# Kernel optimization log

Hardware: AMD Instinct MI355X
Metric: run time of the kernel (lower is better)

The kernel has to match this reference:

```python
import jax, jax.numpy as jnp
import numpy as np

Q_HEADS, KV_HEADS, HEAD_SIZE, H, MAX_LEN = 16, 4, 64, 1024, 4096
B, S = 1, 4096


def _rope_tables(max_len, head_size):
    half = head_size // 2
    inv_freq = 1.0 / (10000.0 ** (np.arange(half, dtype=np.float32) / half))
    pos = np.arange(max_len, dtype=np.float32)
    ang = pos[:, None] * inv_freq[None, :]  # [max_len, half]
    return jnp.asarray(np.sin(ang)), jnp.asarray(np.cos(ang))


def setup_inputs() -> dict:
    key = jax.random.key(0)
    ks = jax.random.split(key, 6)
    sc = 1.0 / np.sqrt(H)
    x = jax.random.normal(ks[0], (B, S, H), dtype=jnp.float32)
    wq = jax.random.normal(ks[1], (H, H), dtype=jnp.float32) * sc
    wk = jax.random.normal(ks[2], (H, KV_HEADS * HEAD_SIZE), dtype=jnp.float32) * sc
    wv = jax.random.normal(ks[3], (H, KV_HEADS * HEAD_SIZE), dtype=jnp.float32) * sc
    wo = jax.random.normal(ks[4], (H, H), dtype=jnp.float32) * sc
    sin, cos = _rope_tables(MAX_LEN, HEAD_SIZE)
    full_mask = jnp.tril(jnp.ones((MAX_LEN, MAX_LEN), dtype=bool))
    attention_mask = jnp.ones((B, S), dtype=jnp.int32)
    return {"x": x, "attention_mask": attention_mask, "start": 0,
            "wq": wq, "wk": wk, "wv": wv, "wo": wo,
            "sin": sin, "cos": cos, "full_mask": full_mask}


def _rotate(t, sin, cos, start):
    # t: [b, heads, s, head_size]; interleaved even/odd RoPE
    s = t.shape[2]
    sn = sin[start:start + s, :][None, None, :, :]
    cs = cos[start:start + s, :][None, None, :, :]
    even, odd = t[..., 0::2], t[..., 1::2]
    out_even = cs * even - sn * odd
    out_odd = sn * even + cs * odd
    return jnp.stack((out_even, out_odd), axis=-1).reshape(t.shape)


def _expand_kv(t, group):
    # [b, kv_heads, s, d] -> [b, kv_heads*group, s, d]
    b, kvh, s, d = t.shape
    return jnp.broadcast_to(t[:, :, None], (b, kvh, group, s, d)).reshape(b, kvh * group, s, d)


def reference(x, attention_mask, start, wq, wk, wv, wo, sin, cos, full_mask):
    b, s, _ = x.shape
    group = Q_HEADS // KV_HEADS
    Q = (x @ wq).reshape(b, s, Q_HEADS, HEAD_SIZE).transpose(0, 2, 1, 3)
    K = (x @ wk).reshape(b, s, KV_HEADS, HEAD_SIZE).transpose(0, 2, 1, 3)
    V = (x @ wv).reshape(b, s, KV_HEADS, HEAD_SIZE).transpose(0, 2, 1, 3)
    Q = _rotate(Q, sin, cos, start)
    K = _rotate(K, sin, cos, start)
    K = _expand_kv(K, group)
    V = _expand_kv(V, group)
    z = jnp.einsum('bhqd,bhkd->bhqk', Q, K) / (HEAD_SIZE ** 0.5)
    kv_len = start + s
    mask = full_mask[:s, :kv_len][None, None, :, :]
    amask = (attention_mask[:, :kv_len] != 0)[:, None, None, :]
    mask = mask & amask
    z = jnp.where(mask, z, -1000000.0)
    A = jax.nn.softmax(z, axis=-1)
    ctx = jnp.einsum('bhqk,bhkd->bhqd', A, V)
    q_mask = attention_mask[:, :s].astype(ctx.dtype)[:, None, :, None]
    ctx = ctx * q_mask
    ctx = ctx.transpose(0, 2, 1, 3).reshape(b, s, H)
    return ctx @ wo
```

## Files before the change

kernel.cpp:

```cpp
#include <hip/hip_runtime.h>

typedef __bf16 bf16x8 __attribute__((ext_vector_type(8)));
typedef float f32x4 __attribute__((ext_vector_type(4)));
typedef unsigned int u32x4 __attribute__((ext_vector_type(4)));

typedef const void __attribute__((address_space(1)))* gas1;
typedef void __attribute__((address_space(3)))* las3;

__device__ __forceinline__ unsigned short f2bf(float f) {
  unsigned int u = __builtin_bit_cast(unsigned int, f);
  u += 0x7fffu + ((u >> 16) & 1u);
  return (unsigned short)(u >> 16);
}
__device__ __forceinline__ float bf2f(unsigned short h) {
  unsigned int u = ((unsigned int)h) << 16;
  return __builtin_bit_cast(float, u);
}
__device__ __forceinline__ unsigned int pack2bf(float lo, float hi) {
  return (unsigned int)f2bf(lo) | ((unsigned int)f2bf(hi) << 16);
}
__device__ __forceinline__ unsigned int packtr(float lo, float hi) {
  return __builtin_amdgcn_perm(__builtin_bit_cast(unsigned int, hi),
                               __builtin_bit_cast(unsigned int, lo), 0x07060302u);
}

__global__ __launch_bounds__(256) void prep(const float* __restrict__ x,
                                            const float* __restrict__ wq,
                                            const float* __restrict__ wk,
                                            const float* __restrict__ wv,
                                            const float* __restrict__ wo,
                                            const float* __restrict__ sinT,
                                            const float* __restrict__ cosT,
                                            unsigned short* __restrict__ xb,
                                            unsigned short* __restrict__ wtqkv,
                                            unsigned short* __restrict__ wot,
                                            float2* __restrict__ scT) {
  __shared__ float tile[32][33];
  const int b = blockIdx.x;
  const int tid = threadIdx.x;
  if (b < 4096) {
    int i = b * 256 + tid;
    float4 v = ((const float4*)x)[i];
    uint2 o;
    o.x = pack2bf(v.x, v.y);
    o.y = pack2bf(v.z, v.w);
    ((uint2*)xb)[i] = o;
    return;
  }
  if (b >= 6656) {
    int idx = (b - 6656) * 256 + tid;
    scT[idx] = make_float2(sinT[idx], cosT[idx]);
    return;
  }
  const float* src;
  unsigned short* dst;
  int R, C, t;
  if (b < 5120)      { t = b - 4096; src = wq; dst = wtqkv;               R = 1024; C = 1024; }
  else if (b < 5376) { t = b - 5120; src = wk; dst = wtqkv + 1024 * 1024; R = 1024; C = 256; }
  else if (b < 5632) { t = b - 5376; src = wv; dst = wtqkv + 1280 * 1024; R = 1024; C = 256; }
  else               { t = b - 5632; src = wo; dst = wot;                 R = 1024; C = 1024; }
  const int ntc = C >> 5;
  const int c0 = (t % ntc) * 32, r0 = (t / ntc) * 32;
  const int tx = tid & 31, ty = tid >> 5;
#pragma unroll
  for (int i = 0; i < 4; ++i)
    tile[ty + i * 8][tx] = src[(r0 + ty + i * 8) * C + c0 + tx];
  __syncthreads();
#pragma unroll
  for (int i = 0; i < 4; ++i)
    dst[(c0 + ty + i * 8) * R + r0 + tx] = f2bf(tile[tx][ty + i * 8]);
}


__device__ __forceinline__ void stage_tile(const unsigned short* __restrict__ src,
                                           unsigned short* lds, int tid) {
  const int w = tid >> 6;
  const int l = tid & 63;
  const int rsub = l >> 3;
  const int cblk = l & 7;
#pragma unroll
  for (int i = 0; i < 4; ++i) {
    const int row = i * 32 + w * 8 + rsub;
    const int scol = (cblk ^ (row & 7)) * 8;
    __builtin_amdgcn_global_load_lds((gas1)(const void*)&src[(size_t)row * 1024 + scol],
                                     (las3)(void*)&lds[(i * 32 + w * 8) * 64], 16, 0, 0);
  }
}

#define GEMM_STEP(CUR, NXT, KNEXT, DO_STAGE)                                          \
  {                                                                                   \
    if (DO_STAGE) {                                                                   \
      stage_tile(Ab + (KNEXT), sm[NXT][0], tid);                                      \
      stage_tile(Bb + (KNEXT), sm[NXT][1], tid);                                      \
    }                                                                                 \
    const char* As = (const char*)sm[CUR][0];                                         \
    const char* Bs = (const char*)sm[CUR][1];                                         \
    bf16x8 af[2][4], bfr[2][4];                                                       \
    _Pragma("unroll")                                                                 \
    for (int kk = 0; kk < 2; ++kk) {                                                  \
      const int co = (kk * 64 + lgrp * 16) ^ xorsel;                                  \
      _Pragma("unroll")                                                               \
      for (int mi = 0; mi < 4; ++mi)                                                  \
        af[kk][mi] = __builtin_bit_cast(bf16x8,                                       \
            *(const u32x4*)(As + arow + mi * 2048 + co));                             \
      _Pragma("unroll")                                                               \
      for (int ni = 0; ni < 4; ++ni)                                                  \
        bfr[kk][ni] = __builtin_bit_cast(bf16x8,                                      \
            *(const u32x4*)(Bs + brow + ni * 2048 + co));                             \
    }                                                                                 \
    _Pragma("unroll")                                                                 \
    for (int kk = 0; kk < 2; ++kk)                                                    \
      _Pragma("unroll")                                                               \
      for (int mi = 0; mi < 4; ++mi)                                                  \
        _Pragma("unroll")                                                             \
        for (int ni = 0; ni < 4; ++ni)                                                \
          acc[mi][ni] = __builtin_amdgcn_mfma_f32_16x16x32_bf16(af[kk][mi],           \
                            bfr[kk][ni], acc[mi][ni], 0, 0, 0);                       \
    __syncthreads();                                                                  \
  }

__global__ __launch_bounds__(256, 2) void gemm_qkv(const unsigned short* __restrict__ A,
                                                   const unsigned short* __restrict__ Bt,
                                                   const float2* __restrict__ scT,
                                                   unsigned short* __restrict__ Qh,
                                                   unsigned short* __restrict__ Kh,
                                                   unsigned short* __restrict__ Vt) {
  __shared__ __align__(16) unsigned short sm[2][2][128 * 64];
  const int tid = threadIdx.x;
  const int bid = blockIdx.x;
  const int swz = (bid & 7) * 48 + (bid >> 3);
  const int nt = swz % 12, mt = swz / 12;
  const int m0 = mt * 128, n0 = nt * 128;

  const int lane = tid & 63, wid = tid >> 6;
  const int wr = wid >> 1, wc = wid & 1;
  const int lgrp = lane >> 4, lmod = lane & 15;
  const int xorsel = (lmod & 7) << 4;
  const int arow = (wr * 64 + lmod) * 128;
  const int brow = (wc * 64 + lmod) * 128;

  const unsigned short* Ab = A + (size_t)m0 * 1024;
  const unsigned short* Bb = Bt + (size_t)n0 * 1024;

  f32x4 acc[4][4] = {};

  stage_tile(Ab, sm[0][0], tid);
  stage_tile(Bb, sm[0][1], tid);
  __syncthreads();

  for (int t = 0; t < 16; t += 2) {
    GEMM_STEP(0, 1, (size_t)(t + 1) * 64, true);
    GEMM_STEP(1, 0, (size_t)(t + 2) * 64, t < 14);
  }

  const int ncol0 = n0 + wc * 64;
  if (ncol0 >= 1280) {
    const int kvh = (ncol0 - 1280) >> 6;
#pragma unroll
    for (int mi = 0; mi < 4; ++mi)
#pragma unroll
      for (int ni = 0; ni < 4; ++ni) {
        int d = ni * 16 + lmod;
        int s = m0 + wr * 64 + mi * 16 + lgrp * 4;
        uint2 o;
        o.x = pack2bf(acc[mi][ni][0], acc[mi][ni][1]);
        o.y = pack2bf(acc[mi][ni][2], acc[mi][ni][3]);
        *(uint2*)&Vt[((size_t)(kvh * 64 + d)) * 4096 + s] = o;
      }
    return;
  }

  const float qscale = 0.18033688011112042f;
  const bool isQ = (ncol0 < 1024);
  const int h = isQ ? (ncol0 >> 6) : ((ncol0 - 1024) >> 6);
  unsigned short* dstbase = isQ ? Qh : Kh;
  const bool evn = (lmod & 1) == 0;
#pragma unroll
  for (int mi = 0; mi < 4; ++mi)
#pragma unroll
    for (int ni = 0; ni < 4; ++ni) {
      int d = ni * 16 + lmod;
      int i = d >> 1;
#pragma unroll
      for (int r = 0; r < 4; ++r) {
        float v = acc[mi][ni][r];
        float pp = __shfl_xor(v, 1, 64);
        int row = m0 + wr * 64 + mi * 16 + lgrp * 4 + r;
        float2 sc = scT[(size_t)row * 32 + i];
        float e = evn ? v : pp, o = evn ? pp : v;
        float outv = evn ? (sc.y * e - sc.x * o) : (sc.x * e + sc.y * o);
        if (isQ) outv *= qscale;
        dstbase[((size_t)h * 4096 + row) * 64 + d] = f2bf(outv);
      }
    }
}

__global__ __launch_bounds__(256, 2) void gemm_out(const unsigned short* __restrict__ A,
                                                   const unsigned short* __restrict__ Bt,
                                                   float* __restrict__ Cout) {
  __shared__ __align__(16) unsigned short sm[2][2][128 * 64];
  const int tid = threadIdx.x;
  const int bid = blockIdx.x;
  const int swz = (bid & 7) * 32 + (bid >> 3);
  const int nt = swz & 7, mt = swz >> 3;
  const int m0 = mt * 128, n0 = nt * 128;

  const int lane = tid & 63, wid = tid >> 6;
  const int wr = wid >> 1, wc = wid & 1;
  const int lgrp = lane >> 4, lmod = lane & 15;
  const int xorsel = (lmod & 7) << 4;
  const int arow = (wr * 64 + lmod) * 128;
  const int brow = (wc * 64 + lmod) * 128;

  const unsigned short* Ab = A + (size_t)m0 * 1024;
  const unsigned short* Bb = Bt + (size_t)n0 * 1024;

  f32x4 acc[4][4] = {};

  stage_tile(Ab, sm[0][0], tid);
  stage_tile(Bb, sm[0][1], tid);
  __syncthreads();

  for (int t = 0; t < 16; t += 2) {
    GEMM_STEP(0, 1, (size_t)(t + 1) * 64, true);
    GEMM_STEP(1, 0, (size_t)(t + 2) * 64, t < 14);
  }

#pragma unroll
  for (int mi = 0; mi < 4; ++mi)
#pragma unroll
    for (int ni = 0; ni < 4; ++ni)
#pragma unroll
      for (int r = 0; r < 4; ++r) {
        int row = m0 + wr * 64 + mi * 16 + lgrp * 4 + r;
        int col = n0 + wc * 64 + ni * 16 + lmod;
        Cout[(size_t)row * 1024 + col] = acc[mi][ni][r];
      }
}

__global__ __launch_bounds__(256, 4) void attn6(const unsigned short* __restrict__ Qh,
                                                const unsigned short* __restrict__ Kh,
                                                const unsigned short* __restrict__ Vt,
                                                unsigned short* __restrict__ ctx) {
  __shared__ __align__(16) unsigned short Kls[128 * 64];
  __shared__ __align__(16) unsigned short Vls[64 * 128];
  const int bx = blockIdx.x;
  const int head = bx & 15;
  const int qidx = bx >> 4;
  const int qh = (qidx < 32) ? (63 - qidx) : (qidx - 32);
  const int kvh = head >> 2;
  const int tid = threadIdx.x;
  const int wave = tid >> 6, lane = tid & 63;
  const int lgrp = lane >> 4, lmod = lane & 15;
  const int qbase = qh * 64;
  const int ntile = qh >> 1;

  const unsigned short* Kg = Kh + (size_t)kvh * 4096 * 64;
  const unsigned short* Vg = Vt + (size_t)kvh * 64 * 4096;

  const int qrow = qbase + wave * 16 + lmod;
  const unsigned short* Qg = Qh + ((size_t)head * 4096 + qrow) * 64;
  bf16x8 qf0 = __builtin_bit_cast(bf16x8, *(const u32x4*)&Qg[lgrp * 8]);
  bf16x8 qf1 = __builtin_bit_cast(bf16x8, *(const u32x4*)&Qg[32 + lgrp * 8]);

  f32x4 accO[4] = {};
  float m_i = -3e38f, l_i = 0.f;

  for (int kc = 0; kc <= ntile; ++kc) {
    const int kb = kc * 128;
    __syncthreads();
#pragma unroll
    for (int i = 0; i < 4; ++i) {
      int ii = tid + i * 256;
      int r = ii >> 3, b = ii & 7;
      __builtin_amdgcn_global_load_lds(
          (gas1)(const void*)&Kg[(size_t)(kb + r) * 64 + ((b ^ (r & 7)) * 8)],
          (las3)(void*)&Kls[(size_t)ii * 8], 16, 0, 0);
    }
#pragma unroll
    for (int i = 0; i < 4; ++i) {
      int ii = tid + i * 256;
      int d = ii >> 4, b = ii & 15;
      __builtin_amdgcn_global_load_lds(
          (gas1)(const void*)&Vg[(size_t)d * 4096 + kb + ((b ^ (d & 15)) * 8)],
          (las3)(void*)&Vls[(size_t)ii * 8], 16, 0, 0);
    }
    __syncthreads();

    f32x4 s[4][2];
    __builtin_amdgcn_s_setprio(1);
#pragma unroll
    for (int g = 0; g < 4; ++g)
#pragma unroll
      for (int t = 0; t < 2; ++t) {
        const int row = 32 * g + t + 2 * lmod;
        bf16x8 alo = __builtin_bit_cast(bf16x8,
            *(const u32x4*)&Kls[(size_t)row * 64 + ((lgrp ^ (row & 7)) * 8)]);
        bf16x8 ahi = __builtin_bit_cast(bf16x8,
            *(const u32x4*)&Kls[(size_t)row * 64 + (((4 + lgrp) ^ (row & 7)) * 8)]);
        f32x4 z = {};
        z = __builtin_amdgcn_mfma_f32_16x16x32_bf16(alo, qf0, z, 0, 0, 0);
        z = __builtin_amdgcn_mfma_f32_16x16x32_bf16(ahi, qf1, z, 0, 0, 0);
        s[g][t] = z;
      }
    __builtin_amdgcn_s_setprio(0);

    if (kb + 127 > qbase + wave * 16) {
#pragma unroll
      for (int g = 0; g < 4; ++g)
#pragma unroll
        for (int t = 0; t < 2; ++t)
#pragma unroll
          for (int r = 0; r < 4; ++r) {
            int key = kb + 32 * g + 8 * lgrp + 2 * r + t;
            if (key > qrow) s[g][t][r] = -3e38f;
          }
    }

    {
      f32x4 v0 = s[0][0], v1 = s[0][1];
#pragma unroll
      for (int g = 1; g < 4; ++g)
#pragma unroll
        for (int r = 0; r < 4; ++r) {
          v0[r] = fmaxf(v0[r], s[g][0][r]);
          v1[r] = fmaxf(v1[r], s[g][1][r]);
        }
      float mx = fmaxf(fmaxf(fmaxf(v0[0], v0[1]), fmaxf(v0[2], v0[3])),
                       fmaxf(fmaxf(v1[0], v1[1]), fmaxf(v1[2], v1[3])));
      mx = fmaxf(mx, __shfl_xor(mx, 16, 64));
      mx = fmaxf(mx, __shfl_xor(mx, 32, 64));
      float mnew = fmaxf(m_i, mx);
      float alpha = __builtin_amdgcn_exp2f(m_i - mnew);
      m_i = mnew;
      f32x4 su = {};
#pragma unroll
      for (int g = 0; g < 4; ++g)
#pragma unroll
        for (int t = 0; t < 2; ++t)
#pragma unroll
          for (int r = 0; r < 4; ++r) {
            float ev = __builtin_amdgcn_exp2f(s[g][t][r] - mnew);
            s[g][t][r] = ev;
            su[r] += ev;
          }
      float rs = (su[0] + su[1]) + (su[2] + su[3]);
      rs += __shfl_xor(rs, 16, 64);
      rs += __shfl_xor(rs, 32, 64);
      l_i = l_i * alpha + rs;
#pragma unroll
      for (int dt = 0; dt < 4; ++dt)
#pragma unroll
        for (int r = 0; r < 4; ++r) accO[dt][r] *= alpha;
    }

    __builtin_amdgcn_s_setprio(1);
#pragma unroll
    for (int g = 0; g < 4; ++g) {
      u32x4 pk;
      pk[0] = packtr(s[g][0][0], s[g][1][0]);
      pk[1] = packtr(s[g][0][1], s[g][1][1]);
      pk[2] = packtr(s[g][0][2], s[g][1][2]);
      pk[3] = packtr(s[g][0][3], s[g][1][3]);
      bf16x8 pf = __builtin_bit_cast(bf16x8, pk);
#pragma unroll
      for (int dt = 0; dt < 4; ++dt) {
        const int d = dt * 16 + lmod;
        bf16x8 vf = __builtin_bit_cast(bf16x8,
            *(const u32x4*)&Vls[(size_t)d * 128 + (((4 * g + lgrp) ^ lmod) * 8)]);
        accO[dt] = __builtin_amdgcn_mfma_f32_16x16x32_bf16(vf, pf, accO[dt], 0, 0, 0);
      }
    }
    __builtin_amdgcn_s_setprio(0);
  }

  {
    float inv = 1.f / l_i;
#pragma unroll
    for (int dt = 0; dt < 4; ++dt) {
      uint2 o;
      o.x = pack2bf(accO[dt][0] * inv, accO[dt][1] * inv);
      o.y = pack2bf(accO[dt][2] * inv, accO[dt][3] * inv);
      *(uint2*)&ctx[(size_t)qrow * 1024 + head * 64 + dt * 16 + lgrp * 4] = o;
    }
  }
}

extern "C" void kernel_launch(void* const* d_in, const int* in_sizes, int n_in,
                              void* d_out, int out_size, void* d_ws, size_t ws_size,
                              hipStream_t stream) {
  const float* x    = (const float*)d_in[0];
  const float* wq   = (const float*)d_in[3];
  const float* wk   = (const float*)d_in[4];
  const float* wv   = (const float*)d_in[5];
  const float* wo   = (const float*)d_in[6];
  const float* sinT = (const float*)d_in[7];
  const float* cosT = (const float*)d_in[8];

  unsigned short* ws    = (unsigned short*)d_ws;
  unsigned short* xb    = ws;
  unsigned short* wtqkv = xb + 4096 * 1024;
  unsigned short* wot   = wtqkv + 1536 * 1024;
  unsigned short* Qh    = wot + 1024 * 1024;
  unsigned short* Kh    = Qh + 16 * 4096 * 64;
  unsigned short* Vt    = Kh + 4 * 4096 * 64;
  unsigned short* ctx   = Vt + 4 * 64 * 4096;
  float2* scT           = (float2*)(ctx + 4096 * 1024);
  float* out = (float*)d_out;

  prep<<<7168, 256, 0, stream>>>(x, wq, wk, wv, wo, sinT, cosT, xb, wtqkv, wot, scT);
  gemm_qkv<<<384, 256, 0, stream>>>(xb, wtqkv, scT, Qh, Kh, Vt);
  attn6<<<dim3(1024), 256, 0, stream>>>(Qh, Kh, Vt, ctx);
  gemm_out<<<256, 256, 0, stream>>>(ctx, wot, out);
}
```

Before: 216.2 us.

## Split causal attention across two KV halves with a combine pass

Adds an attention kernel that uses 128-row query tiles and splits each tile's causal key range into two halves handled by separate blocks. Each block writes unnormalized partial outputs plus row max and sum to fp32 workspace, and a new combine kernel merges the two halves and writes bf16 context. The aim is to balance per-block work and raise parallelism for the long causal tiles. The cost is an extra kernel launch and extra fp32 partial traffic through global memory. The old path is kept as a fallback when the workspace is too small.

```diff
diff --git a/kernel.cpp b/kernel.cpp
--- a/kernel.cpp
+++ b/kernel.cpp
@@ -11,10 +11,6 @@
   unsigned int u = __builtin_bit_cast(unsigned int, f);
   u += 0x7fffu + ((u >> 16) & 1u);
   return (unsigned short)(u >> 16);
-}
-__device__ __forceinline__ float bf2f(unsigned short h) {
-  unsigned int u = ((unsigned int)h) << 16;
-  return __builtin_bit_cast(float, u);
 }
 __device__ __forceinline__ unsigned int pack2bf(float lo, float hi) {
   return (unsigned int)f2bf(lo) | ((unsigned int)f2bf(hi) << 16);
@@ -238,6 +234,193 @@
       }
 }
 
+__global__ __launch_bounds__(256, 4) void attn9(const unsigned short* __restrict__ Qh,
+                                                const unsigned short* __restrict__ Kh,
+                                                const unsigned short* __restrict__ Vt,
+                                                float* __restrict__ Pp) {
+  __shared__ __align__(16) unsigned short Kls[128 * 64];
+  __shared__ __align__(16) unsigned short Vls[64 * 128];
+  const int bx = blockIdx.x;
+  const int head = bx & 15;
+  const int qidx = (bx >> 4) & 31;
+  const int half = bx >> 9;
+  const int qb = (qidx < 16) ? (31 - qidx) : (qidx - 16);
+  const int kvh = head >> 2;
+  const int tid = threadIdx.x;
+  const int wid = tid >> 6, lane = tid & 63;
+  const int lgrp = lane >> 4, lmod = lane & 15;
+  const int qbase = qb * 128;
+
+  const int T = qb + 1;
+  const int h0 = (T + 1) >> 1;
+  const int k_begin = half ? h0 : 0;
+  const int k_end   = half ? T : h0;
+
+  const unsigned short* Kg = Kh + (size_t)kvh * 4096 * 64;
+  const unsigned short* Vg = Vt + (size_t)kvh * 64 * 4096;
+
+  int qrow[2];
+  bf16x8 qf[2][2];
+#pragma unroll
+  for (int qt = 0; qt < 2; ++qt) {
+    qrow[qt] = qbase + wid * 32 + qt * 16 + lmod;
+    const unsigned short* Qg = Qh + ((size_t)head * 4096 + qrow[qt]) * 64;
+    qf[qt][0] = __builtin_bit_cast(bf16x8, *(const u32x4*)&Qg[lgrp * 8]);
+    qf[qt][1] = __builtin_bit_cast(bf16x8, *(const u32x4*)&Qg[32 + lgrp * 8]);
+  }
+
+  f32x4 accO[2][4] = {};
+  float m_i[2] = {-3e38f, -3e38f}, l_i[2] = {0.f, 0.f};
+
+  for (int kc = k_begin; kc < k_end; ++kc) {
+    const int kb = kc * 128;
+    __syncthreads();
+#pragma unroll
+    for (int i = 0; i < 4; ++i) {
+      int ii = tid + i * 256;
+      int r = ii >> 3, b = ii & 7;
+      __builtin_amdgcn_global_load_lds(
+          (gas1)(const void*)&Kg[(size_t)(kb + r) * 64 + ((b ^ (r & 7)) * 8)],
+          (las3)(void*)&Kls[(size_t)ii * 8], 16, 0, 0);
+    }
+#pragma unroll
+    for (int i = 0; i < 4; ++i) {
+      int ii = tid + i * 256;
+      int d = ii >> 4, b = ii & 15;
+      __builtin_amdgcn_global_load_lds(
+          (gas1)(const void*)&Vg[(size_t)d * 4096 + kb + ((b ^ (d & 15)) * 8)],
+          (las3)(void*)&Vls[(size_t)ii * 8], 16, 0, 0);
+    }
+    __syncthreads();
+
+    f32x4 s[4][2][2];
+    __builtin_amdgcn_s_setprio(1);
+#pragma unroll
+    for (int g = 0; g < 4; ++g)
+#pragma unroll
+      for (int t = 0; t < 2; ++t) {
+        const int row = 32 * g + t + 2 * lmod;
+        bf16x8 alo = __builtin_bit_cast(bf16x8,
+            *(const u32x4*)&Kls[(size_t)row * 64 + ((lgrp ^ (row & 7)) * 8)]);
+        bf16x8 ahi = __builtin_bit_cast(bf16x8,
+            *(const u32x4*)&Kls[(size_t)row * 64 + (((4 + lgrp) ^ (row & 7)) * 8)]);
+#pragma unroll
+        for (int qt = 0; qt < 2; ++qt) {
+          f32x4 z = {};
+          z = __builtin_amdgcn_mfma_f32_16x16x32_bf16(alo, qf[qt][0], z, 0, 0, 0);
+          z = __builtin_amdgcn_mfma_f32_16x16x32_bf16(ahi, qf[qt][1], z, 0, 0, 0);
+          s[g][t][qt] = z;
+        }
+      }
+    __builtin_amdgcn_s_setprio(0);
+
+#pragma unroll
+    for (int qt = 0; qt < 2; ++qt) {
+      if (kb + 127 > qbase + wid * 32 + qt * 16) {
+#pragma unroll
+        for (int g = 0; g < 4; ++g)
+#pragma unroll
+          for (int t = 0; t < 2; ++t)
+#pragma unroll
+            for (int r = 0; r < 4; ++r) {
+              int key = kb + 32 * g + 8 * lgrp + 2 * r + t;
+              if (key > qrow[qt]) s[g][t][qt][r] = -3e38f;
+            }
+      }
+    }
+
+#pragma unroll
+    for (int qt = 0; qt < 2; ++qt) {
+      f32x4 v0 = s[0][0][qt], v1 = s[0][1][qt];
+#pragma unroll
+      for (int g = 1; g < 4; ++g)
+#pragma unroll
+        for (int r = 0; r < 4; ++r) {
+          v0[r] = fmaxf(v0[r], s[g][0][qt][r]);
+          v1[r] = fmaxf(v1[r], s[g][1][qt][r]);
+        }
+      float mx = fmaxf(fmaxf(fmaxf(v0[0], v0[1]), fmaxf(v0[2], v0[3])),
+                       fmaxf(fmaxf(v1[0], v1[1]), fmaxf(v1[2], v1[3])));
+      mx = fmaxf(mx, __shfl_xor(mx, 16, 64));
+      mx = fmaxf(mx, __shfl_xor(mx, 32, 64));
+      float mnew = fmaxf(m_i[qt], mx);
+      float alpha = __builtin_amdgcn_exp2f(m_i[qt] - mnew);
+      m_i[qt] = mnew;
+      f32x4 su = {};
+#pragma unroll
+      for (int g = 0; g < 4; ++g)
+#pragma unroll
+        for (int t = 0; t < 2; ++t)
+#pragma unroll
+          for (int r = 0; r < 4; ++r) {
+            float ev = __builtin_amdgcn_exp2f(s[g][t][qt][r] - mnew);
+            s[g][t][qt][r] = ev;
+            su[r] += ev;
+          }
+      float rs = (su[0] + su[1]) + (su[2] + su[3]);
+      rs += __shfl_xor(rs, 16, 64);
+      rs += __shfl_xor(rs, 32, 64);
+      l_i[qt] = l_i[qt] * alpha + rs;
+#pragma unroll
+      for (int dt = 0; dt < 4; ++dt)
+#pragma unroll
+        for (int r = 0; r < 4; ++r) accO[qt][dt][r] *= alpha;
+    }
+
+    __builtin_amdgcn_s_setprio(1);
+#pragma unroll
+    for (int g = 0; g < 4; ++g) {
+      bf16x8 pf[2];
+#pragma unroll
+      for (int qt = 0; qt < 2; ++qt) {
+        u32x4 pk;
+        pk[0] = packtr(s[g][0][qt][0], s[g][1][qt][0]);
+        pk[1] = packtr(s[g][0][qt][1], s[g][1][qt][1]);
+        pk[2] = packtr(s[g][0][qt][2], s[g][1][qt][2]);
+        pk[3] = packtr(s[g][0][qt][3], s[g][1][qt][3]);
+        pf[qt] = __builtin_bit_cast(bf16x8, pk);
+      }
+#pragma unroll
+      for (int dt = 0; dt < 4; ++dt) {
+        const int d = dt * 16 + lmod;
+        bf16x8 vf = __builtin_bit_cast(bf16x8,
+            *(const u32x4*)&Vls[(size_t)d * 128 + (((4 * g + lgrp) ^ lmod) * 8)]);
+        accO[0][dt] = __builtin_amdgcn_mfma_f32_16x16x32_bf16(vf, pf[0], accO[0][dt], 0, 0, 0);
+        accO[1][dt] = __builtin_amdgcn_mfma_f32_16x16x32_bf16(vf, pf[1], accO[1][dt], 0, 0, 0);
+      }
+    }
+    __builtin_amdgcn_s_setprio(0);
+  }
+
+  float* base = Pp + ((size_t)(half * 16 + head) * 4096) * 68;
+#pragma unroll
+  for (int qt = 0; qt < 2; ++qt) {
+#pragma unroll
+    for (int dt = 0; dt < 4; ++dt)
+      *(f32x4*)&base[(size_t)qrow[qt] * 68 + dt * 16 + lgrp * 4] = accO[qt][dt];
+    if (lgrp == 0)
+      *(float2*)&base[(size_t)qrow[qt] * 68 + 64] = make_float2(m_i[qt], l_i[qt]);
+  }
+}
+
+__global__ __launch_bounds__(256) void combine(const float* __restrict__ Pp,
+                                               unsigned short* __restrict__ ctx) {
+  const int tid = threadIdx.x;
+  const int hr = blockIdx.x * 4 + (tid >> 6);
+  const int d = tid & 63;
+  const float* p0 = Pp + (size_t)hr * 68;
+  const float* p1 = Pp + ((size_t)(16 * 4096) + hr) * 68;
+  float m0 = p0[64], l0 = p0[65];
+  float m1 = p1[64], l1 = p1[65];
+  float m = fmaxf(m0, m1);
+  float w0 = __builtin_amdgcn_exp2f(m0 - m);
+  float w1 = __builtin_amdgcn_exp2f(m1 - m);
+  float l = w0 * l0 + w1 * l1;
+  float o = (w0 * p0[d] + w1 * p1[d]) / l;
+  const int head = hr >> 12, qrow = hr & 4095;
+  ctx[(size_t)qrow * 1024 + head * 64 + d] = f2bf(o);
+}
+
 __global__ __launch_bounds__(256, 4) void attn6(const unsigned short* __restrict__ Qh,
                                                 const unsigned short* __restrict__ Kh,
                                                 const unsigned short* __restrict__ Vt,
@@ -406,10 +589,18 @@
   unsigned short* Vt    = Kh + 4 * 4096 * 64;
   unsigned short* ctx   = Vt + 4 * 64 * 4096;
   float2* scT           = (float2*)(ctx + 4096 * 1024);
+  float* Pp             = (float*)(scT + 4096 * 32);
   float* out = (float*)d_out;
 
+  const size_t need = 35651584ull  + 2ull * 16 * 4096 * 68 * 4 ;
+
   prep<<<7168, 256, 0, stream>>>(x, wq, wk, wv, wo, sinT, cosT, xb, wtqkv, wot, scT);
-  gemm_qkv<<<384, 256, 0, stream>>>(xb, wtqkv, scT, Qh, Kh, Vt);
-  attn6<<<dim3(1024), 256, 0, stream>>>(Qh, Kh, Vt, ctx);
-  gemm_out<<<256, 256, 0, stream>>>(ctx, wot, out);
-}
+  gemm_qkv<<<dim3(384), 256, 0, stream>>>(xb, wtqkv, scT, Qh, Kh, Vt);
+  if (ws_size >= need) {
+    attn9<<<dim3(1024), 256, 0, stream>>>(Qh, Kh, Vt, Pp);
+    combine<<<dim3(16384), 256, 0, stream>>>(Pp, ctx);
+  } else {
+    attn6<<<dim3(1024), 256, 0, stream>>>(Qh, Kh, Vt, ctx);
+  }
+  gemm_out<<<dim3(256), 256, 0, stream>>>(ctx, wot, out);
+}
```

After: 404.5 us. 87.1% more time.
